# Kernel optimization log

Measured on AMD Instinct MI355X. Metric: run time of the kernel, lower is better.

The kernel has to match this reference:

```python
import jax, jax.numpy as jnp
import numpy as np

N_NODES = 100000
N_EDGES = 1_600_000


def setup_inputs() -> dict:
    key = jax.random.key(0)
    ks = jax.random.split(key, 18)
    glorot = lambda k, fi, fo: jax.random.normal(k, (fi, fo), jnp.float32) * np.sqrt(2.0 / (fi + fo))
    inp = {
        "x": jax.random.normal(ks[0], (N_NODES, 5), jnp.float32),
        "edge_index": jax.random.randint(ks[1], (2, N_EDGES), 0, N_NODES, jnp.int64 if jax.config.jax_enable_x64 else jnp.int32),
        "W1": glorot(ks[2], 5, 32),  "b1": jnp.zeros((32,), jnp.float32),
        "W2": glorot(ks[3], 32, 32), "b2": jnp.zeros((32,), jnp.float32),
        "W3": glorot(ks[4], 32, 32), "b3": jnp.zeros((32,), jnp.float32),
        "Wd": glorot(ks[5], 32, 1),  "bd": jnp.zeros((1,), jnp.float32),
        "Wa": glorot(ks[6], 32, 1),  "ba": jnp.zeros((1,), jnp.float32),
        "Wt": glorot(ks[7], 32, 2),  "bt": jnp.zeros((2,), jnp.float32),
        "Wact": glorot(ks[8], 32, 9), "bact": jnp.zeros((9,), jnp.float32),
    }
    return inp


def _gcn_layer(x, row, col, norm, W, b):
    # GCNConv(add_self_loops=False): out[col] += norm * (x @ W)[row], then + bias
    h = x @ W                                  # [N, F_out]
    msg = h[row] * norm[:, None]               # [E, F_out]
    return jax.ops.segment_sum(msg, col, num_segments=N_NODES) + b


def reference(x, edge_index, W1, b1, W2, b2, W3, b3, Wd, bd, Wa, ba, Wt, bt, Wact, bact):
    row, col = edge_index[0], edge_index[1]
    # symmetric gcn normalization: deg over targets (unit edge weights)
    deg = jax.ops.segment_sum(jnp.ones((row.shape[0],), x.dtype), col, num_segments=N_NODES)
    dis = jnp.where(deg > 0, jax.lax.rsqrt(jnp.maximum(deg, 1.0)), 0.0)
    norm = dis[row] * dis[col]                 # [E]

    h = jax.nn.relu(_gcn_layer(x, row, col, norm, W1, b1))   # dropout = identity (eval)
    h = jax.nn.relu(_gcn_layer(h, row, col, norm, W2, b2))
    h = jax.nn.relu(_gcn_layer(h, row, col, norm, W3, b3))

    distance_scores = (h @ Wd + bd)[:, 0]      # [N]
    attention_scores = (h @ Wa + ba)[:, 0]     # [N]
    target_idx = jnp.argmax(attention_scores)
    h_t = h[target_idx]                        # [32]
    target_location_score = h_t @ Wt + bt      # [2]
    action_logits = h_t @ Wact + bact          # [9]
    return distance_scores, attention_scores, target_location_score, action_logits
```

## Files before the change

### kernel.cpp

```cpp
#include <hip/hip_runtime.h>
#include <hip/hip_fp16.h>
#include <math.h>


#define N_NODES 100000
#define F 32
#define BUCKET 64
#define NB ((N_NODES + BUCKET - 1) / BUCKET)
#define NBLK 256
#define SMAX 1536
#define TBKT 32
#define NGRP 8
#define RPG (NBLK / NGRP)

__global__ void hist_kernel(const int* __restrict__ col, int* __restrict__ counts, int E,
                            int* __restrict__ ticket) {
    __shared__ int hist[NB];
    int tid = threadIdx.x, blk = blockIdx.x;
    if (blk == 0 && tid == 0) *ticket = 0;
    for (int i = tid; i < NB; i += 1024) hist[i] = 0;
    __syncthreads();
    int chunk = (((E + NBLK - 1) / NBLK) + 1) & ~1;
    int beg = blk * chunk;
    int end = beg + chunk; if (end > E) end = E;
    int cnt = end - beg; if (cnt < 0) cnt = 0;
    int pairs = cnt >> 1;
    const int2* c2 = (const int2*)(col + beg);
    for (int p = tid; p < pairs; p += 1024) {
        int2 v = c2[p];
        atomicAdd(&hist[v.x >> 6], 1);
        atomicAdd(&hist[v.y >> 6], 1);
    }
    if ((cnt & 1) && tid == 0) atomicAdd(&hist[col[end - 1] >> 6], 1);
    __syncthreads();
    for (int i = tid; i < NB; i += 1024) counts[(size_t)blk * NB + i] = hist[i];
}

__global__ void scan_kernel(int* __restrict__ counts, int* __restrict__ tot,
                            int* __restrict__ bucket_base, int* __restrict__ rowstart,
                            int* __restrict__ ticket) {
    __shared__ int tile[NBLK][TBKT];
    __shared__ int wtot[NGRP][TBKT];
    int tid = threadIdx.x;
    int g = tid >> 5, bl = tid & 31;
    int b = blockIdx.x * TBKT + bl;
    bool valid = (b < NB);
    int jbase = g * RPG;
    int run = 0;
#pragma unroll
    for (int r = 0; r < RPG; r++) {
        int j = jbase + r;
        int v = valid ? counts[(size_t)j * NB + b] : 0;
        tile[j][bl] = run;
        run += v;
    }
    wtot[g][bl] = run;
    __syncthreads();
    int off = 0;
#pragma unroll
    for (int gg = 0; gg < NGRP; gg++) {
        int w = wtot[gg][bl];
        if (gg < g) off += w;
    }
    if (valid) {
#pragma unroll
        for (int r = 0; r < RPG; r++) {
            int j = jbase + r;
            counts[(size_t)j * NB + b] = tile[j][bl] + off;
        }
        if (g == NGRP - 1) tot[b] = off + run;
    }
    __shared__ int lastflag;
    __threadfence();
    __syncthreads();
    if (tid == 0) lastflag = (atomicAdd(ticket, 1) == (int)gridDim.x - 1);
    __syncthreads();
    if (!lastflag) return;
    __threadfence();
    constexpr int PER = (NB + 255) / 256;
    __shared__ int bsum[256];
    int base = tid * PER;
    int loc[PER];
    int s = 0;
#pragma unroll
    for (int k = 0; k < PER; k++) {
        int idx = base + k;
        int v = (idx < NB) ? tot[idx] : 0;
        loc[k] = s;
        s += v;
    }
    bsum[tid] = s;
    __syncthreads();
    for (int off2 = 1; off2 < 256; off2 <<= 1) {
        int v = (tid >= off2) ? bsum[tid - off2] : 0;
        __syncthreads();
        bsum[tid] += v;
        __syncthreads();
    }
    int excl = bsum[tid] - s;
#pragma unroll
    for (int k = 0; k < PER; k++) {
        int idx = base + k;
        if (idx < NB) bucket_base[idx] = excl + loc[k];
    }
    if (tid == 255) {
        bucket_base[NB] = bsum[255];
        rowstart[N_NODES] = bsum[255];
    }
}

__global__ void scatter_kernel(const int* __restrict__ row, const int* __restrict__ col,
                               const int* __restrict__ counts, const int* __restrict__ bucket_base,
                               unsigned* __restrict__ storage, int E) {
    __shared__ int cur[NB];
    int tid = threadIdx.x, blk = blockIdx.x;
    for (int i = tid; i < NB; i += 1024)
        cur[i] = counts[(size_t)blk * NB + i] + bucket_base[i];
    __syncthreads();
    int chunk = (((E + NBLK - 1) / NBLK) + 1) & ~1;
    int beg = blk * chunk;
    int end = beg + chunk; if (end > E) end = E;
    int cnt = end - beg; if (cnt < 0) cnt = 0;
    int pairs = cnt >> 1;
    const int2* c2 = (const int2*)(col + beg);
    const int2* r2 = (const int2*)(row + beg);
    for (int p = tid; p < pairs; p += 1024) {
        int2 c = c2[p];
        int2 r = r2[p];
        int pos0 = atomicAdd(&cur[c.x >> 6], 1);
        storage[pos0] = ((unsigned)(c.x & 63) << 17) | (unsigned)r.x;
        int pos1 = atomicAdd(&cur[c.y >> 6], 1);
        storage[pos1] = ((unsigned)(c.y & 63) << 17) | (unsigned)r.y;
    }
    if ((cnt & 1) && tid == 0) {
        int c = col[end - 1], r = row[end - 1];
        int pos = atomicAdd(&cur[c >> 6], 1);
        storage[pos] = ((unsigned)(c & 63) << 17) | (unsigned)r;
    }
}

__global__ void csr_build_kernel(const unsigned* __restrict__ storage, const int* __restrict__ bucket_base,
                                 int* __restrict__ rowstart, int* __restrict__ csr_src,
                                 float* __restrict__ dis, const float* __restrict__ x,
                                 float* __restrict__ xd, int n) {
    __shared__ unsigned sh[SMAX];
    __shared__ int outloc[SMAX];
    __shared__ int hist[BUCKET];
    __shared__ int pre[BUCKET];
    __shared__ int cur[BUCKET];
    __shared__ float dloc[BUCKET];
    int b = blockIdx.x, tid = threadIdx.x;
    if (tid < BUCKET) hist[tid] = 0;
    __syncthreads();
    int base = bucket_base[b];
    int tot = bucket_base[b + 1] - base;
    if (tot > SMAX) tot = SMAX;
    for (int i = tid; i < tot; i += 256) sh[i] = storage[base + i];
    __syncthreads();
    for (int i = tid; i < tot; i += 256) atomicAdd(&hist[sh[i] >> 17], 1);
    __syncthreads();
    if (tid < BUCKET) pre[tid] = hist[tid];
    __syncthreads();
    for (int off = 1; off < BUCKET; off <<= 1) {
        int v = 0;
        if (tid < BUCKET && tid >= off) v = pre[tid - off];
        __syncthreads();
        if (tid < BUCKET && tid >= off) pre[tid] += v;
        __syncthreads();
    }
    if (tid < BUCKET) {
        int excl = pre[tid] - hist[tid];
        cur[tid] = excl;
        int node = b * BUCKET + tid;
        if (node < n) {
            rowstart[node] = base + excl;
            int d = hist[tid];
            float dv = (d > 0) ? rsqrtf((float)d) : 0.0f;
            dis[node] = dv;
            dloc[tid] = dv;
        }
    }
    __syncthreads();
    for (int i = tid; i < BUCKET * 8; i += 256) {
        int nl = i >> 3, f = i & 7;
        int node = b * BUCKET + nl;
        if (node < n) xd[(size_t)node * 8 + f] = (f < 5) ? dloc[nl] * x[(size_t)node * 5 + f] : 0.0f;
    }
    for (int i = tid; i < tot; i += 256) {
        unsigned p = sh[i];
        int pos = atomicAdd(&cur[p >> 17], 1);
        outloc[pos] = (int)(p & 0x1FFFF);
    }
    __syncthreads();
    for (int i = tid; i < tot; i += 256) csr_src[base + i] = outloc[i];
}

__global__ void layer1_fused(const float* __restrict__ xd, const int* __restrict__ rowstart,
                             const int* __restrict__ csr_src, const float* __restrict__ dis,
                             const float* __restrict__ W1, const float* __restrict__ b1,
                             __half* __restrict__ gda, int n) {
    __shared__ float Ws[5 * F];
    __shared__ float s1s[32][8];
    int tid = threadIdx.x;
    if (tid < 5 * F) Ws[tid] = W1[tid];
    int grp = tid >> 3, f = tid & 7;
    int node = blockIdx.x * 32 + grp;
    float sum = 0.0f;
    if (node < n) {
        int start = rowstart[node], end = rowstart[node + 1];
        float a0 = 0, a1 = 0, a2 = 0, a3 = 0, a4 = 0, a5 = 0, a6 = 0, a7 = 0;
        int i = start;
        for (; i + 7 < end; i += 8) {
            int r0 = csr_src[i], r1 = csr_src[i+1], r2 = csr_src[i+2], r3 = csr_src[i+3];
            int r4 = csr_src[i+4], r5 = csr_src[i+5], r6 = csr_src[i+6], r7 = csr_src[i+7];
            a0 += xd[r0*8+f]; a1 += xd[r1*8+f]; a2 += xd[r2*8+f]; a3 += xd[r3*8+f];
            a4 += xd[r4*8+f]; a5 += xd[r5*8+f]; a6 += xd[r6*8+f]; a7 += xd[r7*8+f];
        }
        for (; i < end; i++) a0 += xd[csr_src[i]*8+f];
        sum = ((a0+a1)+(a2+a3)) + ((a4+a5)+(a6+a7));
    }
    s1s[grp][f] = sum;
    __syncthreads();
    if (node < n) {
        float dv = dis[node];
        float sk0 = dv * s1s[grp][0], sk1 = dv * s1s[grp][1], sk2 = dv * s1s[grp][2];
        float sk3 = dv * s1s[grp][3], sk4 = dv * s1s[grp][4];
        int fb = f * 4;
#pragma unroll
        for (int j = 0; j < 4; j++) {
            int ff = fb + j;
            float acc = b1[ff] + sk0 * Ws[0*F+ff] + sk1 * Ws[1*F+ff] + sk2 * Ws[2*F+ff]
                       + sk3 * Ws[3*F+ff] + sk4 * Ws[4*F+ff];
            float h = acc > 0.0f ? acc : 0.0f;
            gda[(size_t)node * F + ff] = __float2half(dv * h);
        }
    }
}

__device__ __forceinline__ void gather16(const uint2* __restrict__ gin2,
                                         const int* __restrict__ csr_src,
                                         int start, int end, int l,
                                         float& a0, float& a1, float& a2, float& a3) {
    a0 = a1 = a2 = a3 = 0.0f;
    int i = start;
    if (i + 16 <= end) {
        int i0 = csr_src[i + l];
        int i1 = csr_src[i + 8 + l];
        while (i + 16 <= end) {
            int nexti = i + 16;
            int n0 = 0, n1 = 0;
            if (nexti + 16 <= end) {
                n0 = csr_src[nexti + l];
                n1 = csr_src[nexti + 8 + l];
            }
            uint2 v[16];
#pragma unroll
            for (int j = 0; j < 8; j++) {
                int r = __shfl(i0, j, 8);
                v[j] = gin2[(size_t)r * 8 + l];
            }
#pragma unroll
            for (int j = 0; j < 8; j++) {
                int r = __shfl(i1, j, 8);
                v[8 + j] = gin2[(size_t)r * 8 + l];
            }
#pragma unroll
            for (int j = 0; j < 16; j++) {
                float2 f0 = __half22float2(*(__half2*)&v[j].x);
                float2 f1 = __half22float2(*(__half2*)&v[j].y);
                a0 += f0.x; a1 += f0.y; a2 += f1.x; a3 += f1.y;
            }
            i0 = n0; i1 = n1;
            i = nexti;
        }
    }
    if (i + 8 <= end) {
        int idx = csr_src[i + l];
        uint2 v[8];
#pragma unroll
        for (int j = 0; j < 8; j++) {
            int r = __shfl(idx, j, 8);
            v[j] = gin2[(size_t)r * 8 + l];
        }
#pragma unroll
        for (int j = 0; j < 8; j++) {
            float2 f0 = __half22float2(*(__half2*)&v[j].x);
            float2 f1 = __half22float2(*(__half2*)&v[j].y);
            a0 += f0.x; a1 += f0.y; a2 += f1.x; a3 += f1.y;
        }
        i += 8;
    }
    for (; i < end; i++) {
        int r = csr_src[i];
        uint2 vv = gin2[(size_t)r * 8 + l];
        float2 f0 = __half22float2(*(__half2*)&vv.x);
        float2 f1 = __half22float2(*(__half2*)&vv.y);
        a0 += f0.x; a1 += f0.y; a2 += f1.x; a3 += f1.y;
    }
}

__global__ void layer_mid_fused(const uint2* __restrict__ gin2, const int* __restrict__ rowstart,
                                const int* __restrict__ csr_src, const float* __restrict__ dis,
                                const float* __restrict__ W, const float* __restrict__ bb,
                                uint2* __restrict__ gout2, int n, int E) {
    __shared__ float Ws[F * F];
    __shared__ float hs[32][F + 1];
    int tid = threadIdx.x;
    for (int i = tid; i < F * F; i += 256) Ws[i] = W[i];
    int grp = tid >> 3;
    int l = tid & 7;
    int node = blockIdx.x * 32 + grp;
    int start = rowstart[node], end = rowstart[node + 1];
    float a0, a1, a2, a3;
    gather16(gin2, csr_src, start, end, l, a0, a1, a2, a3);
    float dv = dis[node];
    int fb = 4 * l;
    hs[grp][fb]     = dv * a0;
    hs[grp][fb + 1] = dv * a1;
    hs[grp][fb + 2] = dv * a2;
    hs[grp][fb + 3] = dv * a3;
    __syncthreads();
    float acc0 = bb[fb], acc1 = bb[fb+1], acc2 = bb[fb+2], acc3 = bb[fb+3];
#pragma unroll
    for (int k = 0; k < F; k++) {
        float hv = hs[grp][k];
        acc0 += hv * Ws[k*F+fb];
        acc1 += hv * Ws[k*F+fb+1];
        acc2 += hv * Ws[k*F+fb+2];
        acc3 += hv * Ws[k*F+fb+3];
    }
    float h0 = acc0 > 0.0f ? acc0 : 0.0f;
    float h1 = acc1 > 0.0f ? acc1 : 0.0f;
    float h2 = acc2 > 0.0f ? acc2 : 0.0f;
    float h3 = acc3 > 0.0f ? acc3 : 0.0f;
    __half2 o0 = __floats2half2_rn(dv * h0, dv * h1);
    __half2 o1 = __floats2half2_rn(dv * h2, dv * h3);
    uint2 pack;
    pack.x = *(unsigned*)&o0;
    pack.y = *(unsigned*)&o1;
    gout2[(size_t)node * 8 + l] = pack;
}

__global__ void layer_last_fused(const uint2* __restrict__ gin2, const int* __restrict__ rowstart,
                                 const int* __restrict__ csr_src, const float* __restrict__ dis,
                                 const float* __restrict__ W3, const float* __restrict__ b3,
                                 const float* __restrict__ Wd, const float* __restrict__ bd,
                                 const float* __restrict__ Wa, const float* __restrict__ ba,
                                 float* __restrict__ out, float* __restrict__ pmax,
                                 int* __restrict__ pidx, int n, int E) {
    __shared__ float Ws[F * F];
    __shared__ float hs[32][F + 1];
    __shared__ float gmax[32];
    __shared__ int gidx[32];
    int tid = threadIdx.x;
    for (int i = tid; i < F * F; i += 256) Ws[i] = W3[i];
    int grp = tid >> 3;
    int l = tid & 7;
    int node = blockIdx.x * 32 + grp;
    int start = rowstart[node], end = rowstart[node + 1];
    float a0, a1, a2, a3;
    gather16(gin2, csr_src, start, end, l, a0, a1, a2, a3);
    float dv = dis[node];
    int fb = 4 * l;
    hs[grp][fb]     = dv * a0;
    hs[grp][fb + 1] = dv * a1;
    hs[grp][fb + 2] = dv * a2;
    hs[grp][fb + 3] = dv * a3;
    __syncthreads();
    float acc0 = b3[fb], acc1 = b3[fb+1], acc2 = b3[fb+2], acc3 = b3[fb+3];
#pragma unroll
    for (int k = 0; k < F; k++) {
        float hv = hs[grp][k];
        acc0 += hv * Ws[k*F+fb];
        acc1 += hv * Ws[k*F+fb+1];
        acc2 += hv * Ws[k*F+fb+2];
        acc3 += hv * Ws[k*F+fb+3];
    }
    float h0 = acc0 > 0.0f ? acc0 : 0.0f;
    float h1 = acc1 > 0.0f ? acc1 : 0.0f;
    float h2 = acc2 > 0.0f ? acc2 : 0.0f;
    float h3 = acc3 > 0.0f ? acc3 : 0.0f;
    float dterm = h0 * Wd[fb] + h1 * Wd[fb+1] + h2 * Wd[fb+2] + h3 * Wd[fb+3];
    float aterm = h0 * Wa[fb] + h1 * Wa[fb+1] + h2 * Wa[fb+2] + h3 * Wa[fb+3];
#pragma unroll
    for (int off = 4; off > 0; off >>= 1) {
        dterm += __shfl_xor(dterm, off, 8);
        aterm += __shfl_xor(aterm, off, 8);
    }
    if (l == 0) {
        out[node] = dterm + bd[0];
        float asc = aterm + ba[0];
        out[N_NODES + node] = asc;
        gmax[grp] = asc;
        gidx[grp] = node;
    }
    __syncthreads();
    if (tid == 0) {
        float best = gmax[0]; int bi = gidx[0];
        for (int g = 1; g < 32; g++) {
            if (gmax[g] > best || (gmax[g] == best && gidx[g] < bi)) { best = gmax[g]; bi = gidx[g]; }
        }
        pmax[blockIdx.x] = best;
        pidx[blockIdx.x] = bi;
    }
}

__global__ void final_kernel(const float* __restrict__ pmax, const int* __restrict__ pidx, int nblocks,
                             const __half* __restrict__ gin, const int* __restrict__ rowstart,
                             const int* __restrict__ csr_src, const float* __restrict__ dis,
                             const float* __restrict__ W3, const float* __restrict__ b3,
                             const float* __restrict__ Wt, const float* __restrict__ bt,
                             const float* __restrict__ Wact, const float* __restrict__ bact,
                             float* __restrict__ out) {
    __shared__ float smax[256];
    __shared__ int sidx[256];
    __shared__ float part[8][F];
    __shared__ float hrow[F];
    __shared__ float ht[F];
    int tid = threadIdx.x;
    float best = -INFINITY; int bi = 0x7fffffff;
    for (int i = tid; i < nblocks; i += 256) {
        float v = pmax[i]; int ix = pidx[i];
        if (v > best || (v == best && ix < bi)) { best = v; bi = ix; }
    }
    smax[tid] = best; sidx[tid] = bi;
    __syncthreads();
    for (int st = 128; st > 0; st >>= 1) {
        if (tid < st) {
            float v2 = smax[tid + st]; int i2 = sidx[tid + st];
            if (v2 > smax[tid] || (v2 == smax[tid] && i2 < sidx[tid])) { smax[tid] = v2; sidx[tid] = i2; }
        }
        __syncthreads();
    }
    int target = sidx[0];
    int g = tid >> 5, f = tid & 31;
    int start = rowstart[target], end = rowstart[target + 1];
    float acc = 0.0f;
    for (int i = start + g; i < end; i += 8)
        acc += __half2float(gin[(size_t)csr_src[i] * F + f]);
    part[g][f] = acc;
    __syncthreads();
    if (tid < F) {
        float s = 0.0f;
#pragma unroll
        for (int gg = 0; gg < 8; gg++) s += part[gg][tid];
        hrow[tid] = dis[target] * s;
    }
    __syncthreads();
    if (tid < F) {
        float a = b3[tid];
#pragma unroll
        for (int k = 0; k < F; k++) a += hrow[k] * W3[k*F+tid];
        ht[tid] = a > 0.0f ? a : 0.0f;
    }
    __syncthreads();
    if (tid < 2) {
        float a = bt[tid];
#pragma unroll
        for (int k = 0; k < F; k++) a += ht[k] * Wt[k*2+tid];
        out[2 * N_NODES + tid] = a;
    } else if (tid < 11) {
        int j = tid - 2;
        float a = bact[j];
#pragma unroll
        for (int k = 0; k < F; k++) a += ht[k] * Wact[k*9+j];
        out[2 * N_NODES + 2 + j] = a;
    }
}

extern "C" void kernel_launch(void* const* d_in, const int* in_sizes, int n_in,
                              void* d_out, int out_size, void* d_ws, size_t ws_size,
                              hipStream_t stream) {
    const float* x  = (const float*)d_in[0];
    const int*   ei = (const int*)d_in[1];
    const int E = in_sizes[1] / 2;
    const int* row = ei;
    const int* col = ei + E;
    const float* W1 = (const float*)d_in[2];
    const float* b1 = (const float*)d_in[3];
    const float* W2 = (const float*)d_in[4];
    const float* b2 = (const float*)d_in[5];
    const float* W3 = (const float*)d_in[6];
    const float* b3 = (const float*)d_in[7];
    const float* Wd = (const float*)d_in[8];
    const float* bd = (const float*)d_in[9];
    const float* Wa = (const float*)d_in[10];
    const float* ba = (const float*)d_in[11];
    const float* Wt = (const float*)d_in[12];
    const float* bt = (const float*)d_in[13];
    const float* Wact = (const float*)d_in[14];
    const float* bact = (const float*)d_in[15];

    float* out = (float*)d_out;
    float* ws  = (float*)d_ws;

    float*    dis      = ws;
    float*    xd       = ws + N_NODES;
    __half*   gd_a     = (__half*)(ws + (size_t)17 * N_NODES);
    __half*   gd_b     = (__half*)(ws + (size_t)33 * N_NODES);
    unsigned* storage  = (unsigned*)(ws + (size_t)33 * N_NODES);
    int*      bucket_base = (int*)(ws + (size_t)49 * N_NODES);
    int*      counts   = bucket_base + NB + 1;
    int*      rowstart = counts + NBLK * NB;
    int*      csr_src  = rowstart + N_NODES + 1;
    float*    pmax     = (float*)(csr_src + E);
    int*      pidx     = (int*)(pmax + 12500);
    int*      tot      = pidx + 12500;
    int*      ticket   = tot + NB;

    const int B = 256;
    const int nb32 = (N_NODES + 31) / 32;
    const int nscan = (NB + TBKT - 1) / TBKT;

    hist_kernel<<<NBLK, 1024, 0, stream>>>(col, counts, E, ticket);
    scan_kernel<<<nscan, B, 0, stream>>>(counts, tot, bucket_base, rowstart, ticket);
    scatter_kernel<<<NBLK, 1024, 0, stream>>>(row, col, counts, bucket_base, storage, E);
    csr_build_kernel<<<NB, B, 0, stream>>>(storage, bucket_base, rowstart, csr_src, dis, x, xd, N_NODES);

    layer1_fused<<<nb32, B, 0, stream>>>(xd, rowstart, csr_src, dis, W1, b1, gd_a, N_NODES);

    layer_mid_fused<<<nb32, B, 0, stream>>>((const uint2*)gd_a, rowstart, csr_src, dis,
                                            W2, b2, (uint2*)gd_b, N_NODES, E);

    layer_last_fused<<<nb32, B, 0, stream>>>((const uint2*)gd_b, rowstart, csr_src, dis,
                                             W3, b3, Wd, bd, Wa, ba, out, pmax, pidx, N_NODES, E);
    final_kernel<<<1, B, 0, stream>>>(pmax, pidx, nb32, gd_b, rowstart, csr_src, dis,
                                      W3, b3, Wt, bt, Wact, bact, out);
}
```

Before: 224.3 us.

## Replace bucketed two-level CSR build with direct global-atomic degree count and scatter

The CSR construction no longer uses a per-block bucket histogram, transposed scan, bucket scatter and per-bucket local sort. It now counts node degrees with global atomics, runs a two-kernel prefix scan over nodes, and scatters source indices directly into CSR slots with per-node global atomic cursors. This removes the intermediate storage pass and the large counts matrix, at the cost of about 3.2M global atomics that contend on random addresses. Edge order within each row also becomes nondeterministic.

```diff
diff --git a/kernel.cpp b/kernel.cpp
--- a/kernel.cpp
+++ b/kernel.cpp
@@ -5,71 +5,38 @@
 
 #define N_NODES 100000
 #define F 32
-#define BUCKET 64
-#define NB ((N_NODES + BUCKET - 1) / BUCKET)
-#define NBLK 256
-#define SMAX 1536
-#define TBKT 32
-#define NGRP 8
-#define RPG (NBLK / NGRP)
-
-__global__ void hist_kernel(const int* __restrict__ col, int* __restrict__ counts, int E,
-                            int* __restrict__ ticket) {
-    __shared__ int hist[NB];
+#define NSCB ((N_NODES + 1023) / 1024)
+
+__global__ void zero_kernel(int* __restrict__ deg, int* __restrict__ ticket) {
+    int i = blockIdx.x * 1024 + threadIdx.x;
+    if (i < N_NODES) deg[i] = 0;
+    if (i == 0) *ticket = 0;
+}
+
+__global__ void deg_kernel(const int* __restrict__ col, int* __restrict__ deg, int E) {
+    int pairs = E >> 1;
+    const int2* c2 = (const int2*)col;
+    int stride = gridDim.x * blockDim.x;
+    for (int p = blockIdx.x * blockDim.x + threadIdx.x; p < pairs; p += stride) {
+        int2 c = c2[p];
+        atomicAdd(&deg[c.x], 1);
+        atomicAdd(&deg[c.y], 1);
+    }
+    if ((E & 1) && blockIdx.x == 0 && threadIdx.x == 0) atomicAdd(&deg[col[E - 1]], 1);
+}
+
+__global__ void scanA_kernel(const int* __restrict__ deg, int* __restrict__ blockoff,
+                             int* __restrict__ rowstart, int* __restrict__ ticket) {
+    __shared__ int red[1024];
     int tid = threadIdx.x, blk = blockIdx.x;
-    if (blk == 0 && tid == 0) *ticket = 0;
-    for (int i = tid; i < NB; i += 1024) hist[i] = 0;
-    __syncthreads();
-    int chunk = (((E + NBLK - 1) / NBLK) + 1) & ~1;
-    int beg = blk * chunk;
-    int end = beg + chunk; if (end > E) end = E;
-    int cnt = end - beg; if (cnt < 0) cnt = 0;
-    int pairs = cnt >> 1;
-    const int2* c2 = (const int2*)(col + beg);
-    for (int p = tid; p < pairs; p += 1024) {
-        int2 v = c2[p];
-        atomicAdd(&hist[v.x >> 6], 1);
-        atomicAdd(&hist[v.y >> 6], 1);
-    }
-    if ((cnt & 1) && tid == 0) atomicAdd(&hist[col[end - 1] >> 6], 1);
-    __syncthreads();
-    for (int i = tid; i < NB; i += 1024) counts[(size_t)blk * NB + i] = hist[i];
-}
-
-__global__ void scan_kernel(int* __restrict__ counts, int* __restrict__ tot,
-                            int* __restrict__ bucket_base, int* __restrict__ rowstart,
-                            int* __restrict__ ticket) {
-    __shared__ int tile[NBLK][TBKT];
-    __shared__ int wtot[NGRP][TBKT];
-    int tid = threadIdx.x;
-    int g = tid >> 5, bl = tid & 31;
-    int b = blockIdx.x * TBKT + bl;
-    bool valid = (b < NB);
-    int jbase = g * RPG;
-    int run = 0;
-#pragma unroll
-    for (int r = 0; r < RPG; r++) {
-        int j = jbase + r;
-        int v = valid ? counts[(size_t)j * NB + b] : 0;
-        tile[j][bl] = run;
-        run += v;
-    }
-    wtot[g][bl] = run;
-    __syncthreads();
-    int off = 0;
-#pragma unroll
-    for (int gg = 0; gg < NGRP; gg++) {
-        int w = wtot[gg][bl];
-        if (gg < g) off += w;
-    }
-    if (valid) {
-#pragma unroll
-        for (int r = 0; r < RPG; r++) {
-            int j = jbase + r;
-            counts[(size_t)j * NB + b] = tile[j][bl] + off;
-        }
-        if (g == NGRP - 1) tot[b] = off + run;
-    }
+    int i = blk * 1024 + tid;
+    red[tid] = (i < N_NODES) ? deg[i] : 0;
+    __syncthreads();
+    for (int st = 512; st > 0; st >>= 1) {
+        if (tid < st) red[tid] += red[tid + st];
+        __syncthreads();
+    }
+    if (tid == 0) blockoff[blk] = red[0];
     __shared__ int lastflag;
     __threadfence();
     __syncthreads();
@@ -77,122 +44,66 @@
     __syncthreads();
     if (!lastflag) return;
     __threadfence();
-    constexpr int PER = (NB + 255) / 256;
-    __shared__ int bsum[256];
-    int base = tid * PER;
-    int loc[PER];
-    int s = 0;
-#pragma unroll
-    for (int k = 0; k < PER; k++) {
-        int idx = base + k;
-        int v = (idx < NB) ? tot[idx] : 0;
-        loc[k] = s;
-        s += v;
-    }
-    bsum[tid] = s;
-    __syncthreads();
-    for (int off2 = 1; off2 < 256; off2 <<= 1) {
-        int v = (tid >= off2) ? bsum[tid - off2] : 0;
+    if (tid == 0) {
+        int running = 0;
+        for (int b = 0; b < NSCB; b++) {
+            int t = blockoff[b];
+            blockoff[b] = running;
+            running += t;
+        }
+        rowstart[N_NODES] = running;
+    }
+}
+
+__global__ void scanB_kernel(const int* __restrict__ deg, const int* __restrict__ blockoff,
+                             int* __restrict__ rowstart, int* __restrict__ cur,
+                             float* __restrict__ dis, const float* __restrict__ x,
+                             float* __restrict__ xd) {
+    __shared__ int psum[1024];
+    int tid = threadIdx.x, blk = blockIdx.x;
+    int i = blk * 1024 + tid;
+    int d = (i < N_NODES) ? deg[i] : 0;
+    psum[tid] = d;
+    __syncthreads();
+    for (int off = 1; off < 1024; off <<= 1) {
+        int v = (tid >= off) ? psum[tid - off] : 0;
         __syncthreads();
-        bsum[tid] += v;
+        psum[tid] += v;
         __syncthreads();
     }
-    int excl = bsum[tid] - s;
-#pragma unroll
-    for (int k = 0; k < PER; k++) {
-        int idx = base + k;
-        if (idx < NB) bucket_base[idx] = excl + loc[k];
-    }
-    if (tid == 255) {
-        bucket_base[NB] = bsum[255];
-        rowstart[N_NODES] = bsum[255];
-    }
-}
-
-__global__ void scatter_kernel(const int* __restrict__ row, const int* __restrict__ col,
-                               const int* __restrict__ counts, const int* __restrict__ bucket_base,
-                               unsigned* __restrict__ storage, int E) {
-    __shared__ int cur[NB];
-    int tid = threadIdx.x, blk = blockIdx.x;
-    for (int i = tid; i < NB; i += 1024)
-        cur[i] = counts[(size_t)blk * NB + i] + bucket_base[i];
-    __syncthreads();
-    int chunk = (((E + NBLK - 1) / NBLK) + 1) & ~1;
-    int beg = blk * chunk;
-    int end = beg + chunk; if (end > E) end = E;
-    int cnt = end - beg; if (cnt < 0) cnt = 0;
-    int pairs = cnt >> 1;
-    const int2* c2 = (const int2*)(col + beg);
-    const int2* r2 = (const int2*)(row + beg);
-    for (int p = tid; p < pairs; p += 1024) {
+    if (i < N_NODES) {
+        int pos = blockoff[blk] + psum[tid] - d;
+        rowstart[i] = pos;
+        cur[i] = pos;
+        float dv = (d > 0) ? rsqrtf((float)d) : 0.0f;
+        dis[i] = dv;
+        float x0 = x[(size_t)i * 5 + 0], x1 = x[(size_t)i * 5 + 1], x2 = x[(size_t)i * 5 + 2];
+        float x3 = x[(size_t)i * 5 + 3], x4 = x[(size_t)i * 5 + 4];
+        float* xo = xd + (size_t)i * 8;
+        xo[0] = dv * x0; xo[1] = dv * x1; xo[2] = dv * x2; xo[3] = dv * x3;
+        xo[4] = dv * x4; xo[5] = 0.0f;   xo[6] = 0.0f;   xo[7] = 0.0f;
+    }
+}
+
+__global__ void scatter_direct(const int* __restrict__ row, const int* __restrict__ col,
+                               int* __restrict__ cur, int* __restrict__ csr_src, int E) {
+    int pairs = E >> 1;
+    const int2* c2 = (const int2*)col;
+    const int2* r2 = (const int2*)row;
+    int stride = gridDim.x * blockDim.x;
+    for (int p = blockIdx.x * blockDim.x + threadIdx.x; p < pairs; p += stride) {
         int2 c = c2[p];
         int2 r = r2[p];
-        int pos0 = atomicAdd(&cur[c.x >> 6], 1);
-        storage[pos0] = ((unsigned)(c.x & 63) << 17) | (unsigned)r.x;
-        int pos1 = atomicAdd(&cur[c.y >> 6], 1);
-        storage[pos1] = ((unsigned)(c.y & 63) << 17) | (unsigned)r.y;
-    }
-    if ((cnt & 1) && tid == 0) {
-        int c = col[end - 1], r = row[end - 1];
-        int pos = atomicAdd(&cur[c >> 6], 1);
-        storage[pos] = ((unsigned)(c & 63) << 17) | (unsigned)r;
-    }
-}
-
-__global__ void csr_build_kernel(const unsigned* __restrict__ storage, const int* __restrict__ bucket_base,
-                                 int* __restrict__ rowstart, int* __restrict__ csr_src,
-                                 float* __restrict__ dis, const float* __restrict__ x,
-                                 float* __restrict__ xd, int n) {
-    __shared__ unsigned sh[SMAX];
-    __shared__ int outloc[SMAX];
-    __shared__ int hist[BUCKET];
-    __shared__ int pre[BUCKET];
-    __shared__ int cur[BUCKET];
-    __shared__ float dloc[BUCKET];
-    int b = blockIdx.x, tid = threadIdx.x;
-    if (tid < BUCKET) hist[tid] = 0;
-    __syncthreads();
-    int base = bucket_base[b];
-    int tot = bucket_base[b + 1] - base;
-    if (tot > SMAX) tot = SMAX;
-    for (int i = tid; i < tot; i += 256) sh[i] = storage[base + i];
-    __syncthreads();
-    for (int i = tid; i < tot; i += 256) atomicAdd(&hist[sh[i] >> 17], 1);
-    __syncthreads();
-    if (tid < BUCKET) pre[tid] = hist[tid];
-    __syncthreads();
-    for (int off = 1; off < BUCKET; off <<= 1) {
-        int v = 0;
-        if (tid < BUCKET && tid >= off) v = pre[tid - off];
-        __syncthreads();
-        if (tid < BUCKET && tid >= off) pre[tid] += v;
-        __syncthreads();
-    }
-    if (tid < BUCKET) {
-        int excl = pre[tid] - hist[tid];
-        cur[tid] = excl;
-        int node = b * BUCKET + tid;
-        if (node < n) {
-            rowstart[node] = base + excl;
-            int d = hist[tid];
-            float dv = (d > 0) ? rsqrtf((float)d) : 0.0f;
-            dis[node] = dv;
-            dloc[tid] = dv;
-        }
-    }
-    __syncthreads();
-    for (int i = tid; i < BUCKET * 8; i += 256) {
-        int nl = i >> 3, f = i & 7;
-        int node = b * BUCKET + nl;
-        if (node < n) xd[(size_t)node * 8 + f] = (f < 5) ? dloc[nl] * x[(size_t)node * 5 + f] : 0.0f;
-    }
-    for (int i = tid; i < tot; i += 256) {
-        unsigned p = sh[i];
-        int pos = atomicAdd(&cur[p >> 17], 1);
-        outloc[pos] = (int)(p & 0x1FFFF);
-    }
-    __syncthreads();
-    for (int i = tid; i < tot; i += 256) csr_src[base + i] = outloc[i];
+        int pos0 = atomicAdd(&cur[c.x], 1);
+        csr_src[pos0] = r.x;
+        int pos1 = atomicAdd(&cur[c.y], 1);
+        csr_src[pos1] = r.y;
+    }
+    if ((E & 1) && blockIdx.x == 0 && threadIdx.x == 0) {
+        int c = col[E - 1], r = row[E - 1];
+        int pos = atomicAdd(&cur[c], 1);
+        csr_src[pos] = r;
+    }
 }
 
 __global__ void layer1_fused(const float* __restrict__ xd, const int* __restrict__ rowstart,
@@ -498,24 +409,23 @@
     float*    xd       = ws + N_NODES;
     __half*   gd_a     = (__half*)(ws + (size_t)17 * N_NODES);
     __half*   gd_b     = (__half*)(ws + (size_t)33 * N_NODES);
-    unsigned* storage  = (unsigned*)(ws + (size_t)33 * N_NODES);
-    int*      bucket_base = (int*)(ws + (size_t)49 * N_NODES);
-    int*      counts   = bucket_base + NB + 1;
-    int*      rowstart = counts + NBLK * NB;
+    int*      deg      = (int*)(ws + (size_t)49 * N_NODES);
+    int*      cur      = deg + N_NODES;
+    int*      rowstart = cur + N_NODES;
     int*      csr_src  = rowstart + N_NODES + 1;
     float*    pmax     = (float*)(csr_src + E);
     int*      pidx     = (int*)(pmax + 12500);
-    int*      tot      = pidx + 12500;
-    int*      ticket   = tot + NB;
+    int*      blockoff = pidx + 12500;
+    int*      ticket   = blockoff + NSCB + 1;
 
     const int B = 256;
     const int nb32 = (N_NODES + 31) / 32;
-    const int nscan = (NB + TBKT - 1) / TBKT;
-
-    hist_kernel<<<NBLK, 1024, 0, stream>>>(col, counts, E, ticket);
-    scan_kernel<<<nscan, B, 0, stream>>>(counts, tot, bucket_base, rowstart, ticket);
-    scatter_kernel<<<NBLK, 1024, 0, stream>>>(row, col, counts, bucket_base, storage, E);
-    csr_build_kernel<<<NB, B, 0, stream>>>(storage, bucket_base, rowstart, csr_src, dis, x, xd, N_NODES);
+
+    zero_kernel<<<NSCB, 1024, 0, stream>>>(deg, ticket);
+    deg_kernel<<<2048, B, 0, stream>>>(col, deg, E);
+    scanA_kernel<<<NSCB, 1024, 0, stream>>>(deg, blockoff, rowstart, ticket);
+    scanB_kernel<<<NSCB, 1024, 0, stream>>>(deg, blockoff, rowstart, cur, dis, x, xd);
+    scatter_direct<<<2048, B, 0, stream>>>(row, col, cur, csr_src, E);
 
     layer1_fused<<<nb32, B, 0, stream>>>(xd, rowstart, csr_src, dis, W1, b1, gd_a, N_NODES);
 
```

Measured after the change: 394.7 us. 1.76x slower.
